# Optimization experiments

Measured on AMD Instinct MI355X. Metric: run time of the kernel, lower is better.

Reference implementation:

```python
import jax, jax.numpy as jnp
import numpy as np

B, T, D, H, E, R, M, HID, NB = 8, 832, 1024, 16, 16, 8, 16, 4096, 576
LORA_SCALE = 1.0 / R  # alpha / rank


def _ln(x, g, b, eps=1e-6):
    m = x.mean(-1, keepdims=True)
    v = ((x - m) ** 2).mean(-1, keepdims=True)
    return (x - m) / jnp.sqrt(v + eps) * g + b


def setup_inputs() -> dict:
    key = jax.random.key(0)
    ks = jax.random.split(key, 12)
    sd = 0.02
    return {
        's': jax.random.normal(ks[0], (B, T, D), jnp.float32),
        'attn_mask': jnp.zeros((1, 1, T, T), jnp.float32),
        'g1': jnp.ones((D,), jnp.float32),
        'b1': jnp.zeros((D,), jnp.float32),
        'w_qkv': jax.random.normal(ks[1], (D, 3 * D), jnp.float32) * sd,
        'b_qkv': jnp.zeros((3 * D,), jnp.float32),
        'w_proj': jax.random.normal(ks[2], (D, D), jnp.float32) * sd,
        'b_proj': jnp.zeros((D,), jnp.float32),
        'g2': jnp.ones((D,), jnp.float32),
        'b2': jnp.zeros((D,), jnp.float32),
        'w_fc1': jax.random.normal(ks[3], (D, HID), jnp.float32) * sd,
        'b_fc1': jnp.zeros((HID,), jnp.float32),
        'w_fc2': jax.random.normal(ks[4], (HID, D), jnp.float32) * sd,
        'b_fc2': jnp.zeros((D,), jnp.float32),
        'lora_A': jax.random.normal(ks[5], (E, D, R), jnp.float32) * sd,
        'lora_B': jax.random.normal(ks[6], (E, R, D), jnp.float32) * sd,
        'active_expert_indices': jnp.arange(E, dtype=jnp.int32),
        'num_backbone_tokens': NB,
    }


def reference(s, attn_mask, g1, b1, w_qkv, b_qkv, w_proj, b_proj,
              g2, b2, w_fc1, b_fc1, w_fc2, b_fc2, lora_A, lora_B,
              active_expert_indices, num_backbone_tokens):
    Bb, Tt, Dd = s.shape
    hd = Dd // H
    # --- shared attention ---
    x = _ln(s, g1, b1)
    qkv = (x @ w_qkv + b_qkv).reshape(Bb, Tt, 3, H, hd).transpose(2, 0, 3, 1, 4)
    q, k, v = qkv[0], qkv[1], qkv[2]  # [B,H,T,hd]
    scores = jnp.einsum('bhqd,bhkd->bhqk', q * (hd ** -0.5), k) + attn_mask
    p = jax.nn.softmax(scores, axis=-1)
    o = jnp.einsum('bhqk,bhkd->bhqd', p, v).transpose(0, 2, 1, 3).reshape(Bb, Tt, Dd)
    s = s + (o @ w_proj + b_proj)
    # --- shared MLP ---
    s_norm = _ln(s, g2, b2)
    shared = jax.nn.gelu(s_norm @ w_fc1 + b_fc1, approximate=False) @ w_fc2 + b_fc2
    # --- per-expert LoRA on expert token segment ---
    nb = num_backbone_tokens
    z = s_norm[:, nb:, :].reshape(Bb, -1, M, Dd)  # [B,K,M,D]
    Ak = lora_A[active_expert_indices]            # [K,D,R]
    Bk = lora_B[active_expert_indices]            # [K,R,D]
    down = jnp.einsum('bkmd,kdr->bkmr', z, Ak)
    up = jnp.einsum('bkmr,krd->bkmd', down, Bk) * LORA_SCALE
    shared = shared.at[:, nb:, :].add(up.reshape(Bb, -1, Dd))
    return s + shared
```

## Files before the change

### kernel.cpp

```cpp
#include <hip/hip_runtime.h>
#include <hip/hip_bf16.h>
#include <math.h>

typedef unsigned short u16;
typedef __attribute__((ext_vector_type(8))) short short8;
typedef __attribute__((ext_vector_type(4))) float f32x4;

constexpr int B_ = 8, T_ = 832, D_ = 1024, H_ = 16, HID_ = 4096, NB_ = 576;
constexpr int NT_ = B_ * T_;

__device__ inline u16 f2b(float f) {
    union { float f; unsigned u; } x{f};
    unsigned r = (x.u + 0x7FFFu + ((x.u >> 16) & 1u)) >> 16;
    return (u16)r;
}
__device__ inline float b2f(u16 b) {
    union { unsigned u; float f; } x; x.u = ((unsigned)b) << 16; return x.f;
}

__device__ inline float erf_inl(float x) {
    float ax = fabsf(x);
    float t = __frcp_rn(1.0f + 0.3275911f * ax);
    float p = 1.061405429f;
    p = p * t - 1.453152027f;
    p = p * t + 1.421413741f;
    p = p * t - 0.284496736f;
    p = p * t + 0.254829592f;
    p = p * t;
    float e = 1.0f - p * __expf(-ax * ax);
    return copysignf(e, x);
}

__device__ inline void gload_lds16(const void* g, void* l) {
    __builtin_amdgcn_global_load_lds((const __attribute__((address_space(1))) void*)g,
                                     (__attribute__((address_space(3))) void*)l, 16, 0, 0);
}

__global__ __launch_bounds__(256) void wtrans_kernel(const float* __restrict__ in,
                                                     u16* __restrict__ out, int K, int N) {
    __shared__ u16 tile[32][34];
    int n0 = blockIdx.x * 32, k0 = blockIdx.y * 32;
    int tx = threadIdx.x & 31, ty = threadIdx.x >> 5;
    for (int i = 0; i < 4; i++) {
        int k = k0 + ty + i * 8;
        tile[ty + i * 8][tx] = f2b(in[(size_t)k * N + n0 + tx]);
    }
    __syncthreads();
    for (int i = 0; i < 4; i++) {
        int n = n0 + ty + i * 8;
        out[(size_t)n * K + k0 + tx] = tile[tx][ty + i * 8];
    }
}

__global__ __launch_bounds__(256) void ln_kernel(const float* __restrict__ x,
                                                 const float* __restrict__ g,
                                                 const float* __restrict__ bt,
                                                 u16* __restrict__ out) {
    int row = blockIdx.x, tid = threadIdx.x;
    float4 v = ((const float4*)(x + (size_t)row * D_))[tid];
    float s = v.x + v.y + v.z + v.w;
    float q = v.x * v.x + v.y * v.y + v.z * v.z + v.w * v.w;
    for (int o = 1; o < 64; o <<= 1) { s += __shfl_xor(s, o); q += __shfl_xor(q, o); }
    __shared__ float red[4][2];
    if ((tid & 63) == 0) { red[tid >> 6][0] = s; red[tid >> 6][1] = q; }
    __syncthreads();
    s = red[0][0] + red[1][0] + red[2][0] + red[3][0];
    q = red[0][1] + red[1][1] + red[2][1] + red[3][1];
    float mean = s * (1.0f / D_);
    float var = q * (1.0f / D_) - mean * mean;
    float inv = rsqrtf(fmaxf(var, 0.f) + 1e-6f);
    float4 gv = ((const float4*)g)[tid];
    float4 bv = ((const float4*)bt)[tid];
    u16* orow = out + (size_t)row * D_ + tid * 4;
    orow[0] = f2b((v.x - mean) * inv * gv.x + bv.x);
    orow[1] = f2b((v.y - mean) * inv * gv.y + bv.y);
    orow[2] = f2b((v.z - mean) * inv * gv.z + bv.z);
    orow[3] = f2b((v.w - mean) * inv * gv.w + bv.w);
}

template<int BM, int BN, int WR, int WC, int MODE>
__global__ __launch_bounds__(WR * WC * 64, (WR * WC == 8) ? 2 : 3)
void gemm3(const u16* __restrict__ A, const u16* __restrict__ Bt,
           const float* __restrict__ bias, const float* __restrict__ resid,
           void* __restrict__ outp, int M, int N, int K) {
    constexpr int THREADS = WR * WC * 64;
    constexpr int MF = BM / WR / 16;
    constexpr int NF = BN / WC / 16;
    constexpr int NROWS = BM + BN;
    constexpr int CHUNKS = NROWS * 4 / THREADS;
    constexpr int LDSU = NROWS * 32;
    __shared__ u16 lds_[3 * LDSU];

    int tid = threadIdx.x, l = tid & 63, w = tid >> 6;
    int lrow = l & 15, lgrp = l >> 4;
    int wr = w / WC, wc = w % WC;

    int nwg = gridDim.x * gridDim.y;
    int bid = blockIdx.y * gridDim.x + blockIdx.x;
    int cpx = nwg >> 3;
    int swz = (bid & 7) * cpx + (bid >> 3);
    int bx = swz % gridDim.x, by = swz / gridDim.x;
    int m0 = by * BM, n0 = bx * BN;

    const u16* src[CHUNKS];
    int ldst[CHUNKS];
    for (int i = 0; i < CHUNKS; i++) {
        int c = i * THREADS + tid;
        int lc = (c & ~7) | ((c ^ (c >> 3)) & 7);
        int row = lc >> 2, colu = (lc & 3) * 8;
        src[i] = (row < BM) ? A + (size_t)(m0 + row) * K + colu
                            : Bt + (size_t)(n0 + row - BM) * K + colu;
        ldst[i] = c * 8;
    }

#define STAGE3(bufi, kt)                                                    \
    do {                                                                    \
        int kof = (kt) * 32;                                                \
        u16* bb = lds_ + (bufi) * LDSU;                                     \
        for (int i = 0; i < CHUNKS; i++) gload_lds16(src[i] + kof, bb + ldst[i]); \
    } while (0)

    f32x4 acc[MF][NF];
    for (int m = 0; m < MF; m++) for (int n = 0; n < NF; n++) acc[m][n] = (f32x4){0, 0, 0, 0};

    int aidx[MF], bidx[NF];
    for (int m = 0; m < MF; m++) {
        int row = wr * 64 + m * 16 + lrow;
        aidx[m] = (row * 32 + lgrp * 8) ^ (((row >> 1) & 7) << 3);
    }
    for (int n = 0; n < NF; n++) {
        int row = BM + wc * 64 + n * 16 + lrow;
        bidx[n] = (row * 32 + lgrp * 8) ^ (((row >> 1) & 7) << 3);
    }

    int nkt = K >> 5;
    STAGE3(0, 0);
    STAGE3(1, 1);
    if constexpr (CHUNKS == 3) asm volatile("s_waitcnt vmcnt(3)" ::: "memory");
    else                       asm volatile("s_waitcnt vmcnt(4)" ::: "memory");
    asm volatile("s_barrier" ::: "memory");

    int cur = 0;
    for (int t = 0; t < nkt; ++t) {
        int sb = cur + 2; if (sb >= 3) sb -= 3;
        if (t + 2 < nkt) STAGE3(sb, t + 2);

        const u16* bp = lds_ + cur * LDSU;
        short8 af[MF], bfr[NF];
        for (int m = 0; m < MF; m++) af[m] = *(const short8*)(bp + aidx[m]);
        for (int n = 0; n < NF; n++) bfr[n] = *(const short8*)(bp + bidx[n]);

        __builtin_amdgcn_s_setprio(1);
        for (int m = 0; m < MF; m++)
            for (int n = 0; n < NF; n++)
                acc[m][n] = __builtin_amdgcn_mfma_f32_16x16x32_bf16(af[m], bfr[n], acc[m][n], 0, 0, 0);
        __builtin_amdgcn_s_setprio(0);

        if (t + 2 < nkt) {
            if constexpr (CHUNKS == 3) asm volatile("s_waitcnt vmcnt(3)" ::: "memory");
            else                       asm volatile("s_waitcnt vmcnt(4)" ::: "memory");
        } else if (t + 1 < nkt) {
            asm volatile("s_waitcnt vmcnt(0)" ::: "memory");
        }
        asm volatile("s_barrier" ::: "memory");
        cur = cur + 1; if (cur == 3) cur = 0;
    }
#undef STAGE3

    for (int m = 0; m < MF; m++) {
        int rbase = m0 + wr * 64 + m * 16 + lgrp * 4;
        for (int n = 0; n < NF; n++) {
            int col = n0 + wc * 64 + n * 16 + lrow;
            float bv = bias[col];
            for (int j = 0; j < 4; j++) {
                int row = rbase + j;
                float v = acc[m][n][j] + bv;
                size_t off = (size_t)row * N + col;
                if constexpr (MODE == 0) {
                    ((u16*)outp)[off] = f2b(v);
                } else if constexpr (MODE == 1) {
                    ((float*)outp)[off] = v + resid[off];
                } else {
                    float gl = 0.5f * v * (1.0f + erf_inl(v * 0.70710678118654752f));
                    ((u16*)outp)[off] = f2b(gl);
                }
            }
        }
    }
}

__global__ __launch_bounds__(256) void vtrans_kernel(const u16* __restrict__ qkv,
                                                     u16* __restrict__ vt) {
    __shared__ u16 tile[32][66];
    int bh = blockIdx.y, b = bh >> 4, h = bh & 15;
    int t0 = blockIdx.x * 32;
    int dx = threadIdx.x & 63, ty = threadIdx.x >> 6;
    for (int i = 0; i < 8; i++) {
        int tt = ty * 8 + i;
        tile[tt][dx] = qkv[(size_t)(b * T_ + t0 + tt) * 3072 + 2048 + h * 64 + dx];
    }
    __syncthreads();
    int tx = threadIdx.x & 31, dy = threadIdx.x >> 5;
    for (int i = 0; i < 8; i++) {
        int d = dy * 8 + i;
        vt[((size_t)bh * 64 + d) * T_ + t0 + tx] = tile[tx][d];
    }
}

__global__ __launch_bounds__(256) void attn_kernel(const u16* __restrict__ qkv,
                                                   const u16* __restrict__ vt,
                                                   const float* __restrict__ mask,
                                                   u16* __restrict__ obuf) {
    __shared__ u16 Ks[2][4096];
    __shared__ u16 Vs[2][4096];
    __shared__ u16 Ps[4][1024];
    int qt = blockIdx.x, bh = blockIdx.y, b = bh >> 4, h = bh & 15;
    int tid = threadIdx.x, w = tid >> 6, l = tid & 63;
    int lrow = l & 15, lgrp = l >> 4;

    const u16* qp = qkv + (size_t)(b * T_ + qt * 64 + w * 16 + lrow) * 3072 + h * 64 + lgrp * 8;
    short8 aq0, aq1;
    {
        short8 r0 = *(const short8*)qp;
        short8 r1 = *(const short8*)(qp + 32);
        for (int i = 0; i < 8; i++) {
            aq0[i] = (short)f2b(b2f((u16)r0[i]) * 0.125f);
            aq1[i] = (short)f2b(b2f((u16)r1[i]) * 0.125f);
        }
    }

    int tq0 = qt * 64 + w * 16 + lgrp * 4;
    const float* mrow0 = mask + (size_t)tq0 * T_;

    float m_r[4], l_r[4];
    f32x4 oacc[4];
    for (int j = 0; j < 4; j++) { m_r[j] = -1e30f; l_r[j] = 0.f; }
    for (int n = 0; n < 4; n++) oacc[n] = (f32x4){0, 0, 0, 0};

    int sidx0 = tid, sidx1 = 256 + tid;
    int srow0 = sidx0 >> 3, sp0 = sidx0 & 7;
    int srow1 = sidx1 >> 3, sp1 = sidx1 & 7;
    int se0 = (sp0 ^ (srow0 & 7)) * 8, se1 = (sp1 ^ (srow1 & 7)) * 8;
    const u16* kbase = qkv + (size_t)b * T_ * 3072 + 1024 + h * 64;
    const u16* vbase = vt + (size_t)bh * 64 * T_;

#define STAGE_KV(buf, kk0)                                                          \
    do {                                                                            \
        gload_lds16(kbase + (size_t)((kk0) + srow0) * 3072 + se0, &Ks[buf][(w * 64) * 8]);        \
        gload_lds16(kbase + (size_t)((kk0) + srow1) * 3072 + se1, &Ks[buf][(256 + w * 64) * 8]);  \
        gload_lds16(vbase + (size_t)srow0 * T_ + (kk0) + se0, &Vs[buf][(w * 64) * 8]);            \
        gload_lds16(vbase + (size_t)srow1 * T_ + (kk0) + se1, &Vs[buf][(256 + w * 64) * 8]);      \
    } while (0)

    STAGE_KV(0, 0);
    __syncthreads();
    int cur = 0;
    u16* Pw = Ps[w];
    int swl = lrow & 7;
    int slot0 = (lgrp ^ swl) * 8, slot1 = ((lgrp + 4) ^ swl) * 8;

    for (int kt = 0; kt < 13; ++kt) {
        int kk0 = kt * 64;
        if (kt < 12) STAGE_KV(cur ^ 1, kk0 + 64);

        f32x4 sc[4];
        for (int c = 0; c < 4; c++) sc[c] = (f32x4){0, 0, 0, 0};
        const u16* Kb = Ks[cur];
        __builtin_amdgcn_s_setprio(1);
        for (int c = 0; c < 4; c++) {
            const u16* krow = Kb + (c * 16 + lrow) * 64;
            short8 bk0 = *(const short8*)(krow + slot0);
            short8 bk1 = *(const short8*)(krow + slot1);
            sc[c] = __builtin_amdgcn_mfma_f32_16x16x32_bf16(aq0, bk0, sc[c], 0, 0, 0);
            sc[c] = __builtin_amdgcn_mfma_f32_16x16x32_bf16(aq1, bk1, sc[c], 0, 0, 0);
        }
        __builtin_amdgcn_s_setprio(0);

        int lo3 = lrow & 7, hi = lrow >> 3;
        for (int j = 0; j < 4; j++) {
            const float* mr = mrow0 + (size_t)j * T_ + kk0;
            float s0 = sc[0][j] + mr[lrow];
            float s1 = sc[1][j] + mr[16 + lrow];
            float s2 = sc[2][j] + mr[32 + lrow];
            float s3 = sc[3][j] + mr[48 + lrow];
            float mx = fmaxf(fmaxf(s0, s1), fmaxf(s2, s3));
            mx = fmaxf(mx, __shfl_xor(mx, 1));
            mx = fmaxf(mx, __shfl_xor(mx, 2));
            mx = fmaxf(mx, __shfl_xor(mx, 4));
            mx = fmaxf(mx, __shfl_xor(mx, 8));
            float mnew = fmaxf(m_r[j], mx);
            float scf = __expf(m_r[j] - mnew);
            float p0 = __expf(s0 - mnew), p1 = __expf(s1 - mnew);
            float p2 = __expf(s2 - mnew), p3 = __expf(s3 - mnew);
            float ps = (p0 + p1) + (p2 + p3);
            ps += __shfl_xor(ps, 1); ps += __shfl_xor(ps, 2);
            ps += __shfl_xor(ps, 4); ps += __shfl_xor(ps, 8);
            l_r[j] = l_r[j] * scf + ps;
            m_r[j] = mnew;
            for (int n = 0; n < 4; n++) oacc[n][j] *= scf;
            int row_p = lgrp * 4 + j, swp = row_p & 7;
            u16* pr = Pw + row_p * 64;
            pr[((hi ^ swp) * 8) + lo3]       = f2b(p0);
            pr[(((2 + hi) ^ swp) * 8) + lo3] = f2b(p1);
            pr[(((4 + hi) ^ swp) * 8) + lo3] = f2b(p2);
            pr[(((6 + hi) ^ swp) * 8) + lo3] = f2b(p3);
        }

        short8 ap0 = *(const short8*)&Pw[lrow * 64 + slot0];
        short8 ap1 = *(const short8*)&Pw[lrow * 64 + slot1];
        const u16* Vb = Vs[cur];
        __builtin_amdgcn_s_setprio(1);
        for (int n = 0; n < 4; n++) {
            const u16* vrow = Vb + (n * 16 + lrow) * 64;
            short8 bv0 = *(const short8*)(vrow + slot0);
            short8 bv1 = *(const short8*)(vrow + slot1);
            oacc[n] = __builtin_amdgcn_mfma_f32_16x16x32_bf16(ap0, bv0, oacc[n], 0, 0, 0);
            oacc[n] = __builtin_amdgcn_mfma_f32_16x16x32_bf16(ap1, bv1, oacc[n], 0, 0, 0);
        }
        __builtin_amdgcn_s_setprio(0);

        __syncthreads();
        cur ^= 1;
    }
#undef STAGE_KV

    for (int j = 0; j < 4; j++) {
        float inv = 1.0f / l_r[j];
        int t = tq0 + j;
        for (int n = 0; n < 4; n++)
            obuf[(size_t)(b * T_ + t) * 1024 + h * 64 + n * 16 + lrow] = f2b(oacc[n][j] * inv);
    }
}

__global__ __launch_bounds__(256) void lora_kernel(const u16* __restrict__ snorm,
                                                   const float* __restrict__ lA,
                                                   const float* __restrict__ lB,
                                                   const int* __restrict__ idx,
                                                   float* __restrict__ outp) {
    __shared__ float down[16][8];
    int blk = blockIdx.x, b = blk >> 4, kk = blk & 15;
    int e = idx[kk];
    int tok0 = b * T_ + NB_ + kk * 16;
    int tid = threadIdx.x;
    if (tid < 128) {
        int m = tid >> 3, r = tid & 7;
        const u16* z = snorm + (size_t)(tok0 + m) * D_;
        const float* Ae = lA + (size_t)e * D_ * 8 + r;
        float acc = 0.f;
        for (int d = 0; d < D_; ++d) acc += b2f(z[d]) * Ae[(size_t)d * 8];
        down[m][r] = acc;
    }
    __syncthreads();
    for (int ci = 0; ci < 4; ci++) {
        int col = tid + ci * 256;
        float br[8];
        for (int r = 0; r < 8; r++) br[r] = lB[((size_t)e * 8 + r) * D_ + col];
        for (int m = 0; m < 16; m++) {
            float acc = 0.f;
            for (int r = 0; r < 8; r++) acc += down[m][r] * br[r];
            outp[(size_t)(tok0 + m) * D_ + col] += acc * 0.125f;
        }
    }
}

extern "C" void kernel_launch(void* const* d_in, const int* in_sizes, int n_in,
                              void* d_out, int out_size, void* d_ws, size_t ws_size,
                              hipStream_t stream) {
    const float* s      = (const float*)d_in[0];
    const float* mask   = (const float*)d_in[1];
    const float* g1     = (const float*)d_in[2];
    const float* b1     = (const float*)d_in[3];
    const float* w_qkv  = (const float*)d_in[4];
    const float* b_qkv  = (const float*)d_in[5];
    const float* w_proj = (const float*)d_in[6];
    const float* b_proj = (const float*)d_in[7];
    const float* g2     = (const float*)d_in[8];
    const float* b2     = (const float*)d_in[9];
    const float* w_fc1  = (const float*)d_in[10];
    const float* b_fc1  = (const float*)d_in[11];
    const float* w_fc2  = (const float*)d_in[12];
    const float* b_fc2  = (const float*)d_in[13];
    const float* lA     = (const float*)d_in[14];
    const float* lB     = (const float*)d_in[15];
    const int*   eidx   = (const int*)d_in[16];
    float* out = (float*)d_out;
    char* ws = (char*)d_ws;

    u16*   wqkvT = (u16*)(ws + 0);
    u16*   wprojT= (u16*)(ws + 6291456);
    u16*   wfc1T = (u16*)(ws + 8388608);
    u16*   wfc2T = (u16*)(ws + 16777216);
    float* s1    = (float*)(ws + 25165824);
    u16*   xln   = (u16*)(ws + 52428800);
    u16*   vt    = (u16*)(ws + 66060288);
    u16*   qkv   = (u16*)(ws + 79691776);
    u16*   h     = (u16*)(ws + 66060288);

    wtrans_kernel<<<dim3(3072 / 32, 1024 / 32), 256, 0, stream>>>(w_qkv, wqkvT, 1024, 3072);
    wtrans_kernel<<<dim3(1024 / 32, 1024 / 32), 256, 0, stream>>>(w_proj, wprojT, 1024, 1024);
    wtrans_kernel<<<dim3(4096 / 32, 1024 / 32), 256, 0, stream>>>(w_fc1, wfc1T, 1024, 4096);
    wtrans_kernel<<<dim3(1024 / 32, 4096 / 32), 256, 0, stream>>>(w_fc2, wfc2T, 4096, 1024);

    ln_kernel<<<NT_, 256, 0, stream>>>(s, g1, b1, xln);
    gemm3<128, 256, 2, 4, 0><<<dim3(3072 / 256, NT_ / 128), 512, 0, stream>>>(xln, wqkvT, b_qkv, nullptr, qkv, NT_, 3072, 1024);
    vtrans_kernel<<<dim3(26, 128), 256, 0, stream>>>(qkv, vt);
    attn_kernel<<<dim3(13, 128), 256, 0, stream>>>(qkv, vt, mask, xln);
    gemm3<128, 128, 2, 2, 1><<<dim3(1024 / 128, NT_ / 128), 256, 0, stream>>>(xln, wprojT, b_proj, s, s1, NT_, 1024, 1024);
    ln_kernel<<<NT_, 256, 0, stream>>>(s1, g2, b2, xln);
    gemm3<128, 256, 2, 4, 2><<<dim3(4096 / 256, NT_ / 128), 512, 0, stream>>>(xln, wfc1T, b_fc1, nullptr, h, NT_, 4096, 1024);
    gemm3<128, 128, 2, 2, 1><<<dim3(1024 / 128, NT_ / 128), 256, 0, stream>>>(h, wfc2T, b_fc2, s1, out, NT_, 1024, 4096);
    lora_kernel<<<128, 256, 0, stream>>>(xln, lA, lB, eidx, out);
}
```

Before: 445.1 us.

## Enlarge attention query tile to 128 rows and prefetch mask into registers

```diff
diff --git a/kernel.cpp b/kernel.cpp
--- a/kernel.cpp
+++ b/kernel.cpp
@@ -207,18 +207,20 @@
     }
 }
 
-__global__ __launch_bounds__(256) void attn_kernel(const u16* __restrict__ qkv,
-                                                   const u16* __restrict__ vt,
-                                                   const float* __restrict__ mask,
-                                                   u16* __restrict__ obuf) {
+__global__ __launch_bounds__(512, 4) void attn_kernel(const u16* __restrict__ qkv,
+                                                      const u16* __restrict__ vt,
+                                                      const float* __restrict__ mask,
+                                                      u16* __restrict__ obuf) {
     __shared__ u16 Ks[2][4096];
     __shared__ u16 Vs[2][4096];
-    __shared__ u16 Ps[4][1024];
+    __shared__ u16 Ps[8][1024];
     int qt = blockIdx.x, bh = blockIdx.y, b = bh >> 4, h = bh & 15;
     int tid = threadIdx.x, w = tid >> 6, l = tid & 63;
     int lrow = l & 15, lgrp = l >> 4;
 
-    const u16* qp = qkv + (size_t)(b * T_ + qt * 64 + w * 16 + lrow) * 3072 + h * 64 + lgrp * 8;
+    int qrow = qt * 128 + w * 16 + lrow;
+    int qrc = qrow < T_ ? qrow : T_ - 1;
+    const u16* qp = qkv + (size_t)(b * T_ + qrc) * 3072 + h * 64 + lgrp * 8;
     short8 aq0, aq1;
     {
         short8 r0 = *(const short8*)qp;
@@ -229,31 +231,40 @@
         }
     }
 
-    int tq0 = qt * 64 + w * 16 + lgrp * 4;
-    const float* mrow0 = mask + (size_t)tq0 * T_;
+    int tq0 = qt * 128 + w * 16 + lgrp * 4;
+    bool qvalid = tq0 < T_;
+    const float* mrowp[4];
+#pragma unroll
+    for (int j = 0; j < 4; j++) {
+        int tq = tq0 + j; if (tq >= T_) tq = T_ - 1;
+        mrowp[j] = mask + (size_t)tq * T_;
+    }
 
     float m_r[4], l_r[4];
     f32x4 oacc[4];
     for (int j = 0; j < 4; j++) { m_r[j] = -1e30f; l_r[j] = 0.f; }
     for (int n = 0; n < 4; n++) oacc[n] = (f32x4){0, 0, 0, 0};
 
-    int sidx0 = tid, sidx1 = 256 + tid;
-    int srow0 = sidx0 >> 3, sp0 = sidx0 & 7;
-    int srow1 = sidx1 >> 3, sp1 = sidx1 & 7;
-    int se0 = (sp0 ^ (srow0 & 7)) * 8, se1 = (sp1 ^ (srow1 & 7)) * 8;
+    int srow = tid >> 3, sp = tid & 7;
+    int se = (sp ^ (srow & 7)) * 8;
     const u16* kbase = qkv + (size_t)b * T_ * 3072 + 1024 + h * 64;
     const u16* vbase = vt + (size_t)bh * 64 * T_;
 
-#define STAGE_KV(buf, kk0)                                                          \
-    do {                                                                            \
-        gload_lds16(kbase + (size_t)((kk0) + srow0) * 3072 + se0, &Ks[buf][(w * 64) * 8]);        \
-        gload_lds16(kbase + (size_t)((kk0) + srow1) * 3072 + se1, &Ks[buf][(256 + w * 64) * 8]);  \
-        gload_lds16(vbase + (size_t)srow0 * T_ + (kk0) + se0, &Vs[buf][(w * 64) * 8]);            \
-        gload_lds16(vbase + (size_t)srow1 * T_ + (kk0) + se1, &Vs[buf][(256 + w * 64) * 8]);      \
+#define STAGE_KV(buf, kk0)                                                        \
+    do {                                                                          \
+        gload_lds16(kbase + (size_t)((kk0) + srow) * 3072 + se, &Ks[buf][w * 512]); \
+        gload_lds16(vbase + (size_t)srow * T_ + (kk0) + se, &Vs[buf][w * 512]);     \
     } while (0)
 
+    float mc[16], mn[16];
     STAGE_KV(0, 0);
+#pragma unroll
+    for (int j = 0; j < 4; j++)
+#pragma unroll
+        for (int c = 0; c < 4; c++)
+            mc[j * 4 + c] = mrowp[j][c * 16 + lrow];
     __syncthreads();
+
     int cur = 0;
     u16* Pw = Ps[w];
     int swl = lrow & 7;
@@ -261,7 +272,14 @@
 
     for (int kt = 0; kt < 13; ++kt) {
         int kk0 = kt * 64;
-        if (kt < 12) STAGE_KV(cur ^ 1, kk0 + 64);
+        if (kt < 12) {
+            STAGE_KV(cur ^ 1, kk0 + 64);
+#pragma unroll
+            for (int j = 0; j < 4; j++)
+#pragma unroll
+                for (int c = 0; c < 4; c++)
+                    mn[j * 4 + c] = mrowp[j][kk0 + 64 + c * 16 + lrow];
+        }
 
         f32x4 sc[4];
         for (int c = 0; c < 4; c++) sc[c] = (f32x4){0, 0, 0, 0};
@@ -277,12 +295,12 @@
         __builtin_amdgcn_s_setprio(0);
 
         int lo3 = lrow & 7, hi = lrow >> 3;
+#pragma unroll
         for (int j = 0; j < 4; j++) {
-            const float* mr = mrow0 + (size_t)j * T_ + kk0;
-            float s0 = sc[0][j] + mr[lrow];
-            float s1 = sc[1][j] + mr[16 + lrow];
-            float s2 = sc[2][j] + mr[32 + lrow];
-            float s3 = sc[3][j] + mr[48 + lrow];
+            float s0 = sc[0][j] + mc[j * 4 + 0];
+            float s1 = sc[1][j] + mc[j * 4 + 1];
+            float s2 = sc[2][j] + mc[j * 4 + 2];
+            float s3 = sc[3][j] + mc[j * 4 + 3];
             float mx = fmaxf(fmaxf(s0, s1), fmaxf(s2, s3));
             mx = fmaxf(mx, __shfl_xor(mx, 1));
             mx = fmaxf(mx, __shfl_xor(mx, 2));
@@ -320,15 +338,19 @@
         __builtin_amdgcn_s_setprio(0);
 
         __syncthreads();
+#pragma unroll
+        for (int i = 0; i < 16; i++) mc[i] = mn[i];
         cur ^= 1;
     }
 #undef STAGE_KV
 
-    for (int j = 0; j < 4; j++) {
-        float inv = 1.0f / l_r[j];
-        int t = tq0 + j;
-        for (int n = 0; n < 4; n++)
-            obuf[(size_t)(b * T_ + t) * 1024 + h * 64 + n * 16 + lrow] = f2b(oacc[n][j] * inv);
+    if (qvalid) {
+        for (int j = 0; j < 4; j++) {
+            float inv = 1.0f / l_r[j];
+            int t = tq0 + j;
+            for (int n = 0; n < 4; n++)
+                obuf[(size_t)(b * T_ + t) * 1024 + h * 64 + n * 16 + lrow] = f2b(oacc[n][j] * inv);
+        }
     }
 }
 
@@ -404,7 +426,7 @@
     ln_kernel<<<NT_, 256, 0, stream>>>(s, g1, b1, xln);
     gemm3<128, 256, 2, 4, 0><<<dim3(3072 / 256, NT_ / 128), 512, 0, stream>>>(xln, wqkvT, b_qkv, nullptr, qkv, NT_, 3072, 1024);
     vtrans_kernel<<<dim3(26, 128), 256, 0, stream>>>(qkv, vt);
-    attn_kernel<<<dim3(13, 128), 256, 0, stream>>>(qkv, vt, mask, xln);
+    attn_kernel<<<dim3(7, 128), 512, 0, stream>>>(qkv, vt, mask, xln);
     gemm3<128, 128, 2, 2, 1><<<dim3(1024 / 128, NT_ / 128), 256, 0, stream>>>(xln, wprojT, b_proj, s, s1, NT_, 1024, 1024);
     ln_kernel<<<NT_, 256, 0, stream>>>(s1, g2, b2, xln);
     gemm3<128, 256, 2, 4, 2><<<dim3(4096 / 256, NT_ / 128), 512, 0, stream>>>(xln, wfc1T, b_fc1, nullptr, h, NT_, 4096, 1024);
```

Result: faster. 431.3 us (-3.1%).
